# Kernel tuning notes

Measured on AMD Instinct MI355X. Metric: run time of the kernel, lower is better.

Reference implementation:

```python
import jax, jax.numpy as jnp
import numpy as np

# Model dims
H = 1024          # hidden_size
I = 2048          # intermediate_size
E = 8             # num_experts
IE = I // E       # expert_intermediate_size = 256
V = 100000        # vocab_size
B, S = 8, 2048


def _rowwise_quantize(x):
    """Dynamic per-row int8 quantization (faithful to dynamic_quantize_int8, per_channel=True).
    Returns quantized values kept in float32 (identical values to int8->float cast) and per-row scale."""
    max_vals = jnp.max(jnp.abs(x), axis=-1, keepdims=True)
    scale = jnp.maximum(max_vals / 127.0, 1e-8)
    x_q = jnp.clip(jnp.round(x / scale), -128.0, 127.0)
    return x_q, scale[..., 0]


def _quantize_weight(w):
    """Per-output-channel int8 quantization of a [K, N] weight (as in from_float)."""
    max_vals = jnp.max(jnp.abs(w), axis=0, keepdims=True)      # [1, N]
    scale = jnp.maximum(max_vals / 127.0, 1e-8)
    w_q = jnp.clip(jnp.round(w / scale), -128.0, 127.0).astype(jnp.int8)
    return w_q, scale[0]


def setup_inputs() -> dict:
    key = jax.random.key(0)
    ks = jax.random.split(key, 6)
    hidden_states = jax.random.normal(ks[0], (B, S, H), dtype=jnp.float32)
    token_ids = jax.random.randint(ks[1], (B, S), 0, V, dtype=jnp.int32)

    # Pre-quantized expert weights (int8) with per-output-channel fp32 scales.
    gate_w = jax.random.normal(ks[2], (E, H, IE), dtype=jnp.float32) * 0.02
    up_w = jax.random.normal(ks[3], (E, H, IE), dtype=jnp.float32) * 0.02
    down_w = jax.random.normal(ks[4], (E, IE, H), dtype=jnp.float32) * 0.02
    gate_q, gate_scale = jax.vmap(_quantize_weight)(gate_w)   # [E,H,IE] int8, [E,IE]
    up_q, up_scale = jax.vmap(_quantize_weight)(up_w)         # [E,H,IE] int8, [E,IE]
    down_q, down_scale = jax.vmap(_quantize_weight)(down_w)   # [E,IE,H] int8, [E,H]

    # Deterministic contiguous token->expert mapping (V divisible by E here).
    token_to_expert = jnp.minimum(jnp.arange(V, dtype=jnp.int32) // (V // E), E - 1)

    return {
        "hidden_states": hidden_states,
        "token_ids": token_ids,
        "gate_q": gate_q, "gate_scale": gate_scale,
        "up_q": up_q, "up_scale": up_scale,
        "down_q": down_q, "down_scale": down_scale,
        "token_to_expert": token_to_expert,
    }


def reference(hidden_states, token_ids, gate_q, gate_scale, up_q, up_scale,
              down_q, down_scale, token_to_expert):
    Bh, Sh, Hh = hidden_states.shape
    n_exp = gate_q.shape[0]
    vocab = token_to_expert.shape[0]

    tid = jnp.clip(token_ids, 0, vocab - 1)
    expert_ids = token_to_expert[tid].reshape(-1)             # [T]

    x = hidden_states.reshape(-1, Hh)                          # [T, H]
    # Per-row activation quantization is expert-independent -> do it once for all tokens.
    x_q, x_s = _rowwise_quantize(x)                            # [T,H], [T]

    gq = gate_q.astype(jnp.float32)
    uq = up_q.astype(jnp.float32)
    dq = down_q.astype(jnp.float32)

    out = jnp.zeros_like(x)
    for e in range(n_exp):  # small fixed expert count
        # fused quantize-GEMM: int8 matmul + per-row activation scale + per-col weight scale
        gate = (x_q @ gq[e]) * x_s[:, None] * gate_scale[e][None, :]   # [T, IE]
        up = (x_q @ uq[e]) * x_s[:, None] * up_scale[e][None, :]       # [T, IE]
        inter = jax.nn.silu(gate) * up
        i_q, i_s = _rowwise_quantize(inter)
        o = (i_q @ dq[e]) * i_s[:, None] * down_scale[e][None, :]      # [T, H]
        out = jnp.where((expert_ids == e)[:, None], o, out)
    return out.reshape(Bh, Sh, Hh)
```

## Files before the change

### kernel.cpp

```cpp
#include <hip/hip_runtime.h>
#include <hip/hip_bf16.h>

typedef int   int4v   __attribute__((ext_vector_type(4)));
typedef float float4v __attribute__((ext_vector_type(4)));

#define T_TOK 16384
#define TPAD  16448
#define HD    1024
#define IE    256
#define EN    8
#define VSZ   100000

#define M_OFF 16
#define M_TS1 25
#define M_TS2 34

#define XQ_OFF   0ull
#define IQ_OFF   16842752ull
#define PB1_OFF  21053440ull
#define PB2_OFF  25247744ull
#define PERM_OFF 27344896ull
#define XS_OFF   27410688ull
#define IS_OFF   27476480ull
#define META_OFF 27542272ull
#define BC_OFF   27542528ull
#define BB_OFF   27544576ull

__device__ __forceinline__ void gload16(const void* g, void* l) {
    __builtin_amdgcn_global_load_lds(
        (const __attribute__((address_space(1))) unsigned int*)g,
        (__attribute__((address_space(3))) unsigned int*)l,
        16, 0, 0);
}

__global__ void k_hist(const int* __restrict__ ids, const int* __restrict__ t2e,
                       int* __restrict__ bc) {
    __shared__ int h[EN];
    if (threadIdx.x < EN) h[threadIdx.x] = 0;
    __syncthreads();
    int t = blockIdx.x * 256 + threadIdx.x;
    int id = ids[t]; id = min(max(id, 0), VSZ - 1);
    atomicAdd(&h[t2e[id]], 1);
    __syncthreads();
    if (threadIdx.x < EN) bc[blockIdx.x * EN + threadIdx.x] = h[threadIdx.x];
}

__global__ __launch_bounds__(512) void k_scan(const int* __restrict__ bc,
                                              int* __restrict__ bbase,
                                              int* __restrict__ meta) {
    int e = threadIdx.x >> 6;
    int b = threadIdx.x & 63;
    int c = bc[b * EN + e];
    int inc = c;
    #pragma unroll
    for (int s = 1; s < 64; s <<= 1) {
        int v = __shfl_up(inc, s, 64);
        if (b >= s) inc += v;
    }
    int exc = inc - c;
    __shared__ int tot[EN];
    __shared__ int goff[EN];
    if (b == 63) tot[e] = inc;
    __syncthreads();
    if (threadIdx.x == 0) {
        int off = 0, t1 = 0, t2 = 0;
        meta[M_OFF] = 0; meta[M_TS1] = 0; meta[M_TS2] = 0;
        #pragma unroll
        for (int i = 0; i < EN; ++i) {
            goff[i] = off;
            int cc = tot[i];
            off += cc; t1 += (cc + 63) >> 6; t2 += (cc + 31) >> 5;
            meta[M_OFF + i + 1] = off;
            meta[M_TS1 + i + 1] = t1;
            meta[M_TS2 + i + 1] = t2;
        }
    }
    __syncthreads();
    bbase[b * EN + e] = goff[e] + exc;
}

__global__ void k_assign(const int* __restrict__ ids, const int* __restrict__ t2e,
                         const int* __restrict__ bbase, int* __restrict__ perm) {
    __shared__ int cur[EN];
    if (threadIdx.x < EN) cur[threadIdx.x] = bbase[blockIdx.x * EN + threadIdx.x];
    __syncthreads();
    int t = blockIdx.x * 256 + threadIdx.x;
    int id = ids[t]; id = min(max(id, 0), VSZ - 1);
    int e = t2e[id];
    int slot = atomicAdd(&cur[e], 1);
    perm[slot] = t;
}

__global__ __launch_bounds__(256) void k_repack(const int* __restrict__ gq,
                                                const int* __restrict__ uq,
                                                const int* __restrict__ dq,
                                                signed char* __restrict__ pb1,
                                                signed char* __restrict__ pb2) {
    int idx = blockIdx.x * 256 + threadIdx.x;
    if (idx < 262144) {
        int n = idx & 511, kc = (idx >> 9) & 63, e = idx >> 15;
        const int* src = (n < 256) ? gq + (((size_t)((e << 10) + (kc << 4)) << 8) + n)
                                   : uq + (((size_t)((e << 10) + (kc << 4)) << 8) + (n - 256));
        int4v pk;
        #pragma unroll
        for (int jj = 0; jj < 4; ++jj) {
            int b0 = src[(size_t)(jj * 4 + 0) << 8], b1 = src[(size_t)(jj * 4 + 1) << 8];
            int b2 = src[(size_t)(jj * 4 + 2) << 8], b3 = src[(size_t)(jj * 4 + 3) << 8];
            pk[jj] = (b0 & 255) | ((b1 & 255) << 8) | ((b2 & 255) << 16) | (b3 << 24);
        }
        *(int4v*)(pb1 + ((size_t)((((e << 6) + kc) << 9) + n) << 4)) = pk;
    } else {
        int j = idx - 262144;
        int n = j & 1023, kc = (j >> 10) & 15, e = j >> 14;
        const int* src = dq + (((size_t)((e << 8) + (kc << 4)) << 10) + n);
        int4v pk;
        #pragma unroll
        for (int jj = 0; jj < 4; ++jj) {
            int b0 = src[(size_t)(jj * 4 + 0) << 10], b1 = src[(size_t)(jj * 4 + 1) << 10];
            int b2 = src[(size_t)(jj * 4 + 2) << 10], b3 = src[(size_t)(jj * 4 + 3) << 10];
            pk[jj] = (b0 & 255) | ((b1 & 255) << 8) | ((b2 & 255) << 16) | (b3 << 24);
        }
        *(int4v*)(pb2 + ((size_t)((((e << 4) + kc) << 10) + n) << 4)) = pk;
    }
}

__global__ __launch_bounds__(256) void k_quant(const float* __restrict__ hidden,
                                               const int* __restrict__ perm,
                                               signed char* __restrict__ xq,
                                               float* __restrict__ xs) {
    int w = threadIdx.x >> 6, lane = threadIdx.x & 63;
    int slot = blockIdx.x * 4 + w;
    int token = perm[slot];
    const float* row = hidden + (size_t)token * HD;
    float v[16];
    #pragma unroll
    for (int j = 0; j < 4; ++j) {
        float4v f = *(const float4v*)(row + lane * 16 + j * 4);
        v[j*4+0] = f[0]; v[j*4+1] = f[1]; v[j*4+2] = f[2]; v[j*4+3] = f[3];
    }
    float mx = 0.0f;
    #pragma unroll
    for (int j = 0; j < 16; ++j) mx = fmaxf(mx, fabsf(v[j]));
    #pragma unroll
    for (int s = 1; s < 64; s <<= 1) mx = fmaxf(mx, __shfl_xor(mx, s, 64));
    float sc = fmaxf(mx / 127.0f, 1e-8f);
    if (lane == 0) xs[slot] = sc;
    int4v pk;
    #pragma unroll
    for (int j = 0; j < 4; ++j) {
        int b[4];
        #pragma unroll
        for (int u = 0; u < 4; ++u) {
            float t = rintf(v[j*4+u] / sc);
            t = fminf(fmaxf(t, -128.0f), 127.0f);
            b[u] = (int)t;
        }
        pk[j] = (b[0] & 255) | ((b[1] & 255) << 8) | ((b[2] & 255) << 16) | (b[3] << 24);
    }
    *(int4v*)(xq + (size_t)slot * HD + lane * 16) = pk;
}

__global__ __launch_bounds__(256, 2) void k_gemm1(const signed char* __restrict__ xq,
                                                  const signed char* __restrict__ pb1,
                                                  const float* __restrict__ xs,
                                                  const float* __restrict__ gsc,
                                                  const float* __restrict__ usc,
                                                  const int* __restrict__ meta,
                                                  signed char* __restrict__ iq,
                                                  float* __restrict__ isc) {
    int b = blockIdx.x;
    int e = -1, m0 = 0, gend = 0;
    #pragma unroll
    for (int i = 0; i < EN; ++i) {
        int s0 = meta[M_TS1 + i], s1 = meta[M_TS1 + i + 1];
        if (b >= s0 && b < s1) { e = i; m0 = meta[M_OFF + i] + ((b - s0) << 6); gend = meta[M_OFF + i + 1]; }
    }
    if (e < 0) return;
    const int w = threadIdx.x >> 6, lane = threadIdx.x & 63;
    const int q = lane >> 4, r = lane & 15;

    __shared__ signed char lB[2][32768];
    __shared__ signed char lA[2][4096];
    __shared__ float pmax[4][64];
    __shared__ float rsc[64];

    const signed char* pbe = pb1 + (size_t)e * (64 * 512 * 16);
    const int arow = (w << 4) + (lane >> 2);
    const int acq  = (lane & 3) ^ ((lane >> 2) & 3);
    const signed char* ga_base = xq + (size_t)(m0 + arow) * HD + (acq << 4);

    #define G1_STAGE(buf, kt)                                                          \
        {                                                                              \
            int kc0 = (kt) << 2;                                                       \
            _Pragma("unroll")                                                          \
            for (int j = 0; j < 8; ++j) {                                              \
                int n = ((j << 6) + lane) ^ ((w & 1) << 3);                            \
                gload16(pbe + (((size_t)(kc0 + w) * 512 + n) << 4),                    \
                        &lB[buf][((w << 3) + j) << 10]);                               \
            }                                                                          \
            gload16(ga_base + ((kt) << 6), &lA[buf][w << 10]);                         \
        }

    int4v zero = {0, 0, 0, 0};
    int4v accg[4][4], accu[4][4];
    #pragma unroll
    for (int mi = 0; mi < 4; ++mi)
        #pragma unroll
        for (int i = 0; i < 4; ++i) { accg[mi][i] = zero; accu[mi][i] = zero; }

    G1_STAGE(0, 0);
    for (int kt = 0; kt < 16; ++kt) {
        int cur = kt & 1;
        if (kt < 15) G1_STAGE(cur ^ 1, kt + 1);
        __syncthreads();
        int4v a[4];
        #pragma unroll
        for (int mi = 0; mi < 4; ++mi)
            a[mi] = *(const int4v*)&lA[cur][(((mi << 4) + r) << 6) + ((q ^ (r & 3)) << 4)];
        #pragma unroll
        for (int i = 0; i < 4; ++i) {
            int n = (w << 6) + (i << 4) + r;
            int sg = (q << 9) + (n ^ ((q & 1) << 3));
            int su = (q << 9) + ((n + 256) ^ ((q & 1) << 3));
            int4v bg = *(const int4v*)&lB[cur][sg << 4];
            int4v bu = *(const int4v*)&lB[cur][su << 4];
            #pragma unroll
            for (int mi = 0; mi < 4; ++mi) {
                accg[mi][i] = __builtin_amdgcn_mfma_i32_16x16x64_i8(a[mi], bg, accg[mi][i], 0, 0, 0);
                accu[mi][i] = __builtin_amdgcn_mfma_i32_16x16x64_i8(a[mi], bu, accu[mi][i], 0, 0, 0);
            }
        }
        __syncthreads();
    }
    #undef G1_STAGE

    float gs[4], us[4];
    #pragma unroll
    for (int i = 0; i < 4; ++i) {
        int n = (w << 6) + (i << 4) + r;
        gs[i] = gsc[e * IE + n];
        us[i] = usc[e * IE + n];
    }
    float xsr[4][4];
    #pragma unroll
    for (int mi = 0; mi < 4; ++mi)
        #pragma unroll
        for (int g = 0; g < 4; ++g)
            xsr[mi][g] = xs[m0 + mi * 16 + q * 4 + g];

    float inter[4][4][4];
    float pm[4][4];
    #pragma unroll
    for (int mi = 0; mi < 4; ++mi)
        #pragma unroll
        for (int g = 0; g < 4; ++g) {
            float mx = 0.0f;
            #pragma unroll
            for (int i = 0; i < 4; ++i) {
                float gv = (float)accg[mi][i][g] * xsr[mi][g] * gs[i];
                float uv = (float)accu[mi][i][g] * xsr[mi][g] * us[i];
                float sg = gv / (1.0f + expf(-gv));
                float vv = sg * uv;
                inter[mi][i][g] = vv;
                mx = fmaxf(mx, fabsf(vv));
            }
            #pragma unroll
            for (int s = 1; s < 16; s <<= 1) mx = fmaxf(mx, __shfl_xor(mx, s, 64));
            pm[mi][g] = mx;
        }

    if (r == 0) {
        #pragma unroll
        for (int mi = 0; mi < 4; ++mi)
            #pragma unroll
            for (int g = 0; g < 4; ++g)
                pmax[w][mi * 16 + q * 4 + g] = pm[mi][g];
    }
    __syncthreads();
    if (threadIdx.x < 64) {
        int row = threadIdx.x;
        float mx = fmaxf(fmaxf(pmax[0][row], pmax[1][row]), fmaxf(pmax[2][row], pmax[3][row]));
        float sc = fmaxf(mx / 127.0f, 1e-8f);
        rsc[row] = sc;
        if (m0 + row < gend) isc[m0 + row] = sc;
    }
    __syncthreads();
    #pragma unroll
    for (int mi = 0; mi < 4; ++mi)
        #pragma unroll
        for (int g = 0; g < 4; ++g) {
            int row = mi * 16 + q * 4 + g;
            int slot = m0 + row;
            if (slot < gend) {
                float sc = rsc[row];
                #pragma unroll
                for (int i = 0; i < 4; ++i) {
                    float t = rintf(inter[mi][i][g] / sc);
                    t = fminf(fmaxf(t, -128.0f), 127.0f);
                    iq[(size_t)slot * IE + (w << 6) + (i << 4) + r] = (signed char)(int)t;
                }
            }
        }
}

__global__ __launch_bounds__(256, 2) void k_gemm2(const signed char* __restrict__ iq,
                                                  const signed char* __restrict__ pb2,
                                                  const float* __restrict__ isc,
                                                  const float* __restrict__ dsc,
                                                  const int* __restrict__ meta,
                                                  const int* __restrict__ perm,
                                                  float* __restrict__ out) {
    int tile = blockIdx.x >> 1, nh = blockIdx.x & 1;
    int e = -1, m0 = 0, gend = 0;
    #pragma unroll
    for (int i = 0; i < EN; ++i) {
        int s0 = meta[M_TS2 + i], s1 = meta[M_TS2 + i + 1];
        if (tile >= s0 && tile < s1) { e = i; m0 = meta[M_OFF + i] + ((tile - s0) << 5); gend = meta[M_OFF + i + 1]; }
    }
    if (e < 0) return;
    const int w = threadIdx.x >> 6, lane = threadIdx.x & 63;
    const int q = lane >> 4, r = lane & 15;

    __shared__ signed char lB[2][32768];
    __shared__ signed char lA[2][2048];

    const signed char* pbe = pb2 + (size_t)e * (16 * 1024 * 16);
    const int arow = (w << 4) + (lane >> 2);
    const int acq  = (lane & 3) ^ ((lane >> 2) & 3);
    const signed char* ga_base = iq + (size_t)(m0 + arow) * IE + (acq << 4);

    #define G2_STAGE(buf, kt)                                                          \
        {                                                                              \
            int kc0 = (kt) << 2;                                                       \
            _Pragma("unroll")                                                          \
            for (int j = 0; j < 8; ++j) {                                              \
                int n = ((j << 6) + lane) ^ ((w & 1) << 3);                            \
                gload16(pbe + (((size_t)(kc0 + w) * 1024 + (nh << 9) + n) << 4),       \
                        &lB[buf][((w << 3) + j) << 10]);                               \
            }                                                                          \
            if (w < 2) gload16(ga_base + ((kt) << 6), &lA[buf][w << 10]);              \
        }

    int4v zero = {0, 0, 0, 0};
    int4v acc[2][8];
    #pragma unroll
    for (int mi = 0; mi < 2; ++mi)
        #pragma unroll
        for (int i = 0; i < 8; ++i) acc[mi][i] = zero;

    G2_STAGE(0, 0);
    for (int kt = 0; kt < 4; ++kt) {
        int cur = kt & 1;
        if (kt < 3) G2_STAGE(cur ^ 1, kt + 1);
        __syncthreads();
        int4v a[2];
        #pragma unroll
        for (int mi = 0; mi < 2; ++mi)
            a[mi] = *(const int4v*)&lA[cur][(((mi << 4) + r) << 6) + ((q ^ (r & 3)) << 4)];
        #pragma unroll
        for (int i = 0; i < 8; ++i) {
            int n = (w << 7) + (i << 4) + r;
            int sb = (q << 9) + (n ^ ((q & 1) << 3));
            int4v bb = *(const int4v*)&lB[cur][sb << 4];
            acc[0][i] = __builtin_amdgcn_mfma_i32_16x16x64_i8(a[0], bb, acc[0][i], 0, 0, 0);
            acc[1][i] = __builtin_amdgcn_mfma_i32_16x16x64_i8(a[1], bb, acc[1][i], 0, 0, 0);
        }
        __syncthreads();
    }
    #undef G2_STAGE

    float ds[8];
    #pragma unroll
    for (int i = 0; i < 8; ++i)
        ds[i] = dsc[e * HD + (nh << 9) + (w << 7) + (i << 4) + r];
    float isr[2][4]; int tok[2][4];
    #pragma unroll
    for (int mi = 0; mi < 2; ++mi)
        #pragma unroll
        for (int g = 0; g < 4; ++g) {
            int slot = m0 + mi * 16 + q * 4 + g;
            isr[mi][g] = isc[slot];
            tok[mi][g] = perm[slot];
        }
    #pragma unroll
    for (int mi = 0; mi < 2; ++mi)
        #pragma unroll
        for (int g = 0; g < 4; ++g) {
            int slot = m0 + mi * 16 + q * 4 + g;
            if (slot < gend) {
                float vs = isr[mi][g];
                size_t ob = (size_t)tok[mi][g] * HD + (nh << 9) + (w << 7) + r;
                #pragma unroll
                for (int i = 0; i < 8; ++i)
                    out[ob + (i << 4)] = (float)acc[mi][i][g] * vs * ds[i];
            }
        }
}

extern "C" void kernel_launch(void* const* d_in, const int* in_sizes, int n_in,
                              void* d_out, int out_size, void* d_ws, size_t ws_size,
                              hipStream_t stream) {
    const float* hidden = (const float*)d_in[0];
    const int*   ids    = (const int*)d_in[1];
    const int*   gq     = (const int*)d_in[2];
    const float* gsc    = (const float*)d_in[3];
    const int*   uq     = (const int*)d_in[4];
    const float* usc    = (const float*)d_in[5];
    const int*   dq     = (const int*)d_in[6];
    const float* dsc    = (const float*)d_in[7];
    const int*   t2e    = (const int*)d_in[8];
    float* out = (float*)d_out;

    char* ws = (char*)d_ws;
    signed char* xq  = (signed char*)(ws + XQ_OFF);
    signed char* iq  = (signed char*)(ws + IQ_OFF);
    signed char* pb1 = (signed char*)(ws + PB1_OFF);
    signed char* pb2 = (signed char*)(ws + PB2_OFF);
    int*   perm = (int*)(ws + PERM_OFF);
    float* xs   = (float*)(ws + XS_OFF);
    float* isc  = (float*)(ws + IS_OFF);
    int*   meta = (int*)(ws + META_OFF);
    int*   bc   = (int*)(ws + BC_OFF);
    int*   bbase= (int*)(ws + BB_OFF);

    k_hist<<<64, 256, 0, stream>>>(ids, t2e, bc);
    k_scan<<<1, 512, 0, stream>>>(bc, bbase, meta);
    k_assign<<<64, 256, 0, stream>>>(ids, t2e, bbase, perm);
    k_repack<<<1536, 256, 0, stream>>>(gq, uq, dq, pb1, pb2);
    k_quant<<<4096, 256, 0, stream>>>(hidden, perm, xq, xs);
    k_gemm1<<<264, 256, 0, stream>>>(xq, pb1, xs, gsc, usc, meta, iq, isc);
    k_gemm2<<<1040, 256, 0, stream>>>(iq, pb2, isc, dsc, meta, perm, out);
}
```

Measured before the change: 210.0 us.

## Fuse expert GEMMs into one kernel, merge routing and preprocessing launches

```diff
diff --git a/kernel.cpp b/kernel.cpp
--- a/kernel.cpp
+++ b/kernel.cpp
@@ -1,11 +1,9 @@
 #include <hip/hip_runtime.h>
-#include <hip/hip_bf16.h>
 
 typedef int   int4v   __attribute__((ext_vector_type(4)));
 typedef float float4v __attribute__((ext_vector_type(4)));
 
 #define T_TOK 16384
-#define TPAD  16448
 #define HD    1024
 #define IE    256
 #define EN    8
@@ -13,18 +11,13 @@
 
 #define M_OFF 16
 #define M_TS1 25
-#define M_TS2 34
 
 #define XQ_OFF   0ull
-#define IQ_OFF   16842752ull
 #define PB1_OFF  21053440ull
 #define PB2_OFF  25247744ull
 #define PERM_OFF 27344896ull
 #define XS_OFF   27410688ull
-#define IS_OFF   27476480ull
 #define META_OFF 27542272ull
-#define BC_OFF   27542528ull
-#define BB_OFF   27544576ull
 
 __device__ __forceinline__ void gload16(const void* g, void* l) {
     __builtin_amdgcn_global_load_lds(
@@ -33,141 +26,146 @@
         16, 0, 0);
 }
 
-__global__ void k_hist(const int* __restrict__ ids, const int* __restrict__ t2e,
-                       int* __restrict__ bc) {
-    __shared__ int h[EN];
-    if (threadIdx.x < EN) h[threadIdx.x] = 0;
-    __syncthreads();
-    int t = blockIdx.x * 256 + threadIdx.x;
-    int id = ids[t]; id = min(max(id, 0), VSZ - 1);
-    atomicAdd(&h[t2e[id]], 1);
-    __syncthreads();
-    if (threadIdx.x < EN) bc[blockIdx.x * EN + threadIdx.x] = h[threadIdx.x];
+__global__ __launch_bounds__(1024) void k_route(const int* __restrict__ ids,
+                                                const int* __restrict__ t2e,
+                                                int* __restrict__ perm,
+                                                int* __restrict__ meta) {
+    __shared__ int lbase[1024][EN];
+    __shared__ int wsum[16][EN];
+    __shared__ int goff[EN], tot[EN];
+    const int tid = threadIdx.x, lane = tid & 63, wv = tid >> 6;
+
+    #pragma unroll
+    for (int e = 0; e < EN; ++e) lbase[tid][e] = 0;
+    int e_of[16];
+    #pragma unroll
+    for (int i = 0; i < 16; ++i) {
+        int id = ids[tid * 16 + i];
+        id = min(max(id, 0), VSZ - 1);
+        int e = t2e[id];
+        e_of[i] = e;
+        lbase[tid][e]++;
+    }
+    #pragma unroll
+    for (int e = 0; e < EN; ++e) {
+        int v = lbase[tid][e];
+        int inc = v;
+        #pragma unroll
+        for (int s = 1; s < 64; s <<= 1) {
+            int u = __shfl_up(inc, s, 64);
+            if (lane >= s) inc += u;
+        }
+        lbase[tid][e] = inc - v;
+        if (lane == 63) wsum[wv][e] = inc;
+    }
+    __syncthreads();
+    if (tid < EN) {
+        int run = 0;
+        for (int w2 = 0; w2 < 16; ++w2) { int t = wsum[w2][tid]; wsum[w2][tid] = run; run += t; }
+        tot[tid] = run;
+    }
+    __syncthreads();
+    if (tid == 0) {
+        int off = 0, t1 = 0;
+        meta[M_OFF] = 0; meta[M_TS1] = 0;
+        #pragma unroll
+        for (int e = 0; e < EN; ++e) {
+            goff[e] = off;
+            off += tot[e];
+            t1 += (tot[e] + 63) >> 6;
+            meta[M_OFF + e + 1] = off;
+            meta[M_TS1 + e + 1] = t1;
+        }
+    }
+    __syncthreads();
+    #pragma unroll
+    for (int i = 0; i < 16; ++i) {
+        int e = e_of[i];
+        int c = lbase[tid][e];
+        lbase[tid][e] = c + 1;
+        perm[goff[e] + wsum[wv][e] + c] = tid * 16 + i;
+    }
 }
 
-__global__ __launch_bounds__(512) void k_scan(const int* __restrict__ bc,
-                                              int* __restrict__ bbase,
-                                              int* __restrict__ meta) {
-    int e = threadIdx.x >> 6;
-    int b = threadIdx.x & 63;
-    int c = bc[b * EN + e];
-    int inc = c;
-    #pragma unroll
-    for (int s = 1; s < 64; s <<= 1) {
-        int v = __shfl_up(inc, s, 64);
-        if (b >= s) inc += v;
-    }
-    int exc = inc - c;
-    __shared__ int tot[EN];
-    __shared__ int goff[EN];
-    if (b == 63) tot[e] = inc;
-    __syncthreads();
-    if (threadIdx.x == 0) {
-        int off = 0, t1 = 0, t2 = 0;
-        meta[M_OFF] = 0; meta[M_TS1] = 0; meta[M_TS2] = 0;
-        #pragma unroll
-        for (int i = 0; i < EN; ++i) {
-            goff[i] = off;
-            int cc = tot[i];
-            off += cc; t1 += (cc + 63) >> 6; t2 += (cc + 31) >> 5;
-            meta[M_OFF + i + 1] = off;
-            meta[M_TS1 + i + 1] = t1;
-            meta[M_TS2 + i + 1] = t2;
-        }
-    }
-    __syncthreads();
-    bbase[b * EN + e] = goff[e] + exc;
+__global__ __launch_bounds__(256) void k_pre(const float* __restrict__ hidden,
+                                             const int* __restrict__ gq,
+                                             const int* __restrict__ uq,
+                                             const int* __restrict__ dq,
+                                             signed char* __restrict__ xq,
+                                             float* __restrict__ xs,
+                                             signed char* __restrict__ pb1,
+                                             signed char* __restrict__ pb2) {
+    int b = blockIdx.x;
+    if (b < 4096) {
+        int w = threadIdx.x >> 6, lane = threadIdx.x & 63;
+        int token = (b << 2) + w;
+        const float* row = hidden + (size_t)token * HD;
+        float v[16];
+        #pragma unroll
+        for (int j = 0; j < 4; ++j) {
+            float4v f = *(const float4v*)(row + lane * 16 + j * 4);
+            v[j*4+0] = f[0]; v[j*4+1] = f[1]; v[j*4+2] = f[2]; v[j*4+3] = f[3];
+        }
+        float mx = 0.0f;
+        #pragma unroll
+        for (int j = 0; j < 16; ++j) mx = fmaxf(mx, fabsf(v[j]));
+        #pragma unroll
+        for (int s = 1; s < 64; s <<= 1) mx = fmaxf(mx, __shfl_xor(mx, s, 64));
+        float sc = fmaxf(mx / 127.0f, 1e-8f);
+        if (lane == 0) xs[token] = sc;
+        int4v pk;
+        #pragma unroll
+        for (int j = 0; j < 4; ++j) {
+            int bb[4];
+            #pragma unroll
+            for (int u = 0; u < 4; ++u) {
+                float t = rintf(v[j*4+u] / sc);
+                t = fminf(fmaxf(t, -128.0f), 127.0f);
+                bb[u] = (int)t;
+            }
+            pk[j] = (bb[0] & 255) | ((bb[1] & 255) << 8) | ((bb[2] & 255) << 16) | (bb[3] << 24);
+        }
+        *(int4v*)(xq + (size_t)token * HD + lane * 16) = pk;
+    } else {
+        int idx = (b - 4096) * 256 + threadIdx.x;
+        if (idx < 262144) {
+            int n = idx & 511, kc = (idx >> 9) & 63, e = idx >> 15;
+            const int* src = (n < 256) ? gq + (((size_t)((e << 10) + (kc << 4)) << 8) + n)
+                                       : uq + (((size_t)((e << 10) + (kc << 4)) << 8) + (n - 256));
+            int4v pk;
+            #pragma unroll
+            for (int jj = 0; jj < 4; ++jj) {
+                int b0 = src[(size_t)(jj * 4 + 0) << 8], b1 = src[(size_t)(jj * 4 + 1) << 8];
+                int b2 = src[(size_t)(jj * 4 + 2) << 8], b3 = src[(size_t)(jj * 4 + 3) << 8];
+                pk[jj] = (b0 & 255) | ((b1 & 255) << 8) | ((b2 & 255) << 16) | (b3 << 24);
+            }
+            *(int4v*)(pb1 + ((size_t)((((e << 6) + kc) << 9) + n) << 4)) = pk;
+        } else {
+            int j = idx - 262144;
+            int n = j & 1023, kc = (j >> 10) & 15, e = j >> 14;
+            const int* src = dq + (((size_t)((e << 8) + (kc << 4)) << 10) + n);
+            int4v pk;
+            #pragma unroll
+            for (int jj = 0; jj < 4; ++jj) {
+                int b0 = src[(size_t)(jj * 4 + 0) << 10], b1 = src[(size_t)(jj * 4 + 1) << 10];
+                int b2 = src[(size_t)(jj * 4 + 2) << 10], b3 = src[(size_t)(jj * 4 + 3) << 10];
+                pk[jj] = (b0 & 255) | ((b1 & 255) << 8) | ((b2 & 255) << 16) | (b3 << 24);
+            }
+            *(int4v*)(pb2 + ((size_t)((((e << 4) + kc) << 10) + n) << 4)) = pk;
+        }
+    }
 }
 
-__global__ void k_assign(const int* __restrict__ ids, const int* __restrict__ t2e,
-                         const int* __restrict__ bbase, int* __restrict__ perm) {
-    __shared__ int cur[EN];
-    if (threadIdx.x < EN) cur[threadIdx.x] = bbase[blockIdx.x * EN + threadIdx.x];
-    __syncthreads();
-    int t = blockIdx.x * 256 + threadIdx.x;
-    int id = ids[t]; id = min(max(id, 0), VSZ - 1);
-    int e = t2e[id];
-    int slot = atomicAdd(&cur[e], 1);
-    perm[slot] = t;
-}
-
-__global__ __launch_bounds__(256) void k_repack(const int* __restrict__ gq,
-                                                const int* __restrict__ uq,
-                                                const int* __restrict__ dq,
-                                                signed char* __restrict__ pb1,
-                                                signed char* __restrict__ pb2) {
-    int idx = blockIdx.x * 256 + threadIdx.x;
-    if (idx < 262144) {
-        int n = idx & 511, kc = (idx >> 9) & 63, e = idx >> 15;
-        const int* src = (n < 256) ? gq + (((size_t)((e << 10) + (kc << 4)) << 8) + n)
-                                   : uq + (((size_t)((e << 10) + (kc << 4)) << 8) + (n - 256));
-        int4v pk;
-        #pragma unroll
-        for (int jj = 0; jj < 4; ++jj) {
-            int b0 = src[(size_t)(jj * 4 + 0) << 8], b1 = src[(size_t)(jj * 4 + 1) << 8];
-            int b2 = src[(size_t)(jj * 4 + 2) << 8], b3 = src[(size_t)(jj * 4 + 3) << 8];
-            pk[jj] = (b0 & 255) | ((b1 & 255) << 8) | ((b2 & 255) << 16) | (b3 << 24);
-        }
-        *(int4v*)(pb1 + ((size_t)((((e << 6) + kc) << 9) + n) << 4)) = pk;
-    } else {
-        int j = idx - 262144;
-        int n = j & 1023, kc = (j >> 10) & 15, e = j >> 14;
-        const int* src = dq + (((size_t)((e << 8) + (kc << 4)) << 10) + n);
-        int4v pk;
-        #pragma unroll
-        for (int jj = 0; jj < 4; ++jj) {
-            int b0 = src[(size_t)(jj * 4 + 0) << 10], b1 = src[(size_t)(jj * 4 + 1) << 10];
-            int b2 = src[(size_t)(jj * 4 + 2) << 10], b3 = src[(size_t)(jj * 4 + 3) << 10];
-            pk[jj] = (b0 & 255) | ((b1 & 255) << 8) | ((b2 & 255) << 16) | (b3 << 24);
-        }
-        *(int4v*)(pb2 + ((size_t)((((e << 4) + kc) << 10) + n) << 4)) = pk;
-    }
-}
-
-__global__ __launch_bounds__(256) void k_quant(const float* __restrict__ hidden,
-                                               const int* __restrict__ perm,
-                                               signed char* __restrict__ xq,
-                                               float* __restrict__ xs) {
-    int w = threadIdx.x >> 6, lane = threadIdx.x & 63;
-    int slot = blockIdx.x * 4 + w;
-    int token = perm[slot];
-    const float* row = hidden + (size_t)token * HD;
-    float v[16];
-    #pragma unroll
-    for (int j = 0; j < 4; ++j) {
-        float4v f = *(const float4v*)(row + lane * 16 + j * 4);
-        v[j*4+0] = f[0]; v[j*4+1] = f[1]; v[j*4+2] = f[2]; v[j*4+3] = f[3];
-    }
-    float mx = 0.0f;
-    #pragma unroll
-    for (int j = 0; j < 16; ++j) mx = fmaxf(mx, fabsf(v[j]));
-    #pragma unroll
-    for (int s = 1; s < 64; s <<= 1) mx = fmaxf(mx, __shfl_xor(mx, s, 64));
-    float sc = fmaxf(mx / 127.0f, 1e-8f);
-    if (lane == 0) xs[slot] = sc;
-    int4v pk;
-    #pragma unroll
-    for (int j = 0; j < 4; ++j) {
-        int b[4];
-        #pragma unroll
-        for (int u = 0; u < 4; ++u) {
-            float t = rintf(v[j*4+u] / sc);
-            t = fminf(fmaxf(t, -128.0f), 127.0f);
-            b[u] = (int)t;
-        }
-        pk[j] = (b[0] & 255) | ((b[1] & 255) << 8) | ((b[2] & 255) << 16) | (b[3] << 24);
-    }
-    *(int4v*)(xq + (size_t)slot * HD + lane * 16) = pk;
-}
-
-__global__ __launch_bounds__(256, 2) void k_gemm1(const signed char* __restrict__ xq,
-                                                  const signed char* __restrict__ pb1,
-                                                  const float* __restrict__ xs,
-                                                  const float* __restrict__ gsc,
-                                                  const float* __restrict__ usc,
-                                                  const int* __restrict__ meta,
-                                                  signed char* __restrict__ iq,
-                                                  float* __restrict__ isc) {
+__global__ __launch_bounds__(256, 2) void k_mlp(const signed char* __restrict__ xq,
+                                                const signed char* __restrict__ pb1,
+                                                const signed char* __restrict__ pb2,
+                                                const float* __restrict__ xs,
+                                                const float* __restrict__ gsc,
+                                                const float* __restrict__ usc,
+                                                const float* __restrict__ dsc,
+                                                const int* __restrict__ meta,
+                                                const int* __restrict__ perm,
+                                                float* __restrict__ out) {
     int b = blockIdx.x;
     int e = -1, m0 = 0, gend = 0;
     #pragma unroll
@@ -179,15 +177,27 @@
     const int w = threadIdx.x >> 6, lane = threadIdx.x & 63;
     const int q = lane >> 4, r = lane & 15;
 
-    __shared__ signed char lB[2][32768];
-    __shared__ signed char lA[2][4096];
-    __shared__ float pmax[4][64];
-    __shared__ float rsc[64];
-
-    const signed char* pbe = pb1 + (size_t)e * (64 * 512 * 16);
+    __shared__ __align__(16) signed char lB[2][32768];
+    __shared__ __align__(16) signed char arena[16384];
+    float* pmax = (float*)(arena + 8192);
+    float* rsc  = (float*)(arena + 9216);
+    int*   ptok = (int*)(arena + 9472);
+
+    if (threadIdx.x < 64) ptok[threadIdx.x] = perm[min(m0 + (int)threadIdx.x, T_TOK - 1)];
+    __syncthreads();
+
+    int tokr[4][4];
+    #pragma unroll
+    for (int mi = 0; mi < 4; ++mi)
+        #pragma unroll
+        for (int g = 0; g < 4; ++g)
+            tokr[mi][g] = ptok[(mi << 4) + (q << 2) + g];
+
+    const signed char* pbe1 = pb1 + (size_t)e * (64 * 512 * 16);
+    const signed char* pbe2 = pb2 + (size_t)e * (16 * 1024 * 16);
     const int arow = (w << 4) + (lane >> 2);
     const int acq  = (lane & 3) ^ ((lane >> 2) & 3);
-    const signed char* ga_base = xq + (size_t)(m0 + arow) * HD + (acq << 4);
+    const signed char* ga_base = xq + (size_t)ptok[arow] * HD + (acq << 4);
 
     #define G1_STAGE(buf, kt)                                                          \
         {                                                                              \
@@ -195,10 +205,21 @@
             _Pragma("unroll")                                                          \
             for (int j = 0; j < 8; ++j) {                                              \
                 int n = ((j << 6) + lane) ^ ((w & 1) << 3);                            \
-                gload16(pbe + (((size_t)(kc0 + w) * 512 + n) << 4),                    \
+                gload16(pbe1 + (((size_t)(kc0 + w) * 512 + n) << 4),                   \
                         &lB[buf][((w << 3) + j) << 10]);                               \
             }                                                                          \
-            gload16(ga_base + ((kt) << 6), &lA[buf][w << 10]);                         \
+            gload16(ga_base + ((kt) << 6), arena + ((buf) << 12) + (w << 10));         \
+        }
+
+    #define G2_STAGE(buf, st)                                                          \
+        {                                                                              \
+            int kc0 = ((st) & 3) << 2; int nhs = (st) >> 2;                            \
+            _Pragma("unroll")                                                          \
+            for (int j = 0; j < 8; ++j) {                                              \
+                int n = ((j << 6) + lane) ^ ((w & 1) << 3);                            \
+                gload16(pbe2 + (((size_t)(kc0 + w) * 1024 + (nhs << 9) + n) << 4),     \
+                        &lB[buf][((w << 3) + j) << 10]);                               \
+            }                                                                          \
         }
 
     int4v zero = {0, 0, 0, 0};
@@ -216,7 +237,7 @@
         int4v a[4];
         #pragma unroll
         for (int mi = 0; mi < 4; ++mi)
-            a[mi] = *(const int4v*)&lA[cur][(((mi << 4) + r) << 6) + ((q ^ (r & 3)) << 4)];
+            a[mi] = *(const int4v*)&arena[(cur << 12) + ((((mi << 4) + r) << 6) + ((q ^ (r & 3)) << 4))];
         #pragma unroll
         for (int i = 0; i < 4; ++i) {
             int n = (w << 6) + (i << 4) + r;
@@ -234,6 +255,8 @@
     }
     #undef G1_STAGE
 
+    G2_STAGE(0, 0);
+
     float gs[4], us[4];
     #pragma unroll
     for (int i = 0; i < 4; ++i) {
@@ -246,7 +269,7 @@
     for (int mi = 0; mi < 4; ++mi)
         #pragma unroll
         for (int g = 0; g < 4; ++g)
-            xsr[mi][g] = xs[m0 + mi * 16 + q * 4 + g];
+            xsr[mi][g] = xs[tokr[mi][g]];
 
     float inter[4][4][4];
     float pm[4][4];
@@ -274,127 +297,85 @@
         for (int mi = 0; mi < 4; ++mi)
             #pragma unroll
             for (int g = 0; g < 4; ++g)
-                pmax[w][mi * 16 + q * 4 + g] = pm[mi][g];
+                pmax[(w << 6) + (mi << 4) + (q << 2) + g] = pm[mi][g];
     }
     __syncthreads();
     if (threadIdx.x < 64) {
         int row = threadIdx.x;
-        float mx = fmaxf(fmaxf(pmax[0][row], pmax[1][row]), fmaxf(pmax[2][row], pmax[3][row]));
-        float sc = fmaxf(mx / 127.0f, 1e-8f);
-        rsc[row] = sc;
-        if (m0 + row < gend) isc[m0 + row] = sc;
-    }
-    __syncthreads();
+        float mx = fmaxf(fmaxf(pmax[row], pmax[64 + row]), fmaxf(pmax[128 + row], pmax[192 + row]));
+        rsc[row] = fmaxf(mx / 127.0f, 1e-8f);
+    }
+    __syncthreads();
+    float rscr[4][4];
+    #pragma unroll
+    for (int mi = 0; mi < 4; ++mi)
+        #pragma unroll
+        for (int g = 0; g < 4; ++g)
+            rscr[mi][g] = rsc[(mi << 4) + (q << 2) + g];
+    __syncthreads();
+
     #pragma unroll
     for (int mi = 0; mi < 4; ++mi)
         #pragma unroll
         for (int g = 0; g < 4; ++g) {
-            int row = mi * 16 + q * 4 + g;
-            int slot = m0 + row;
-            if (slot < gend) {
-                float sc = rsc[row];
+            int row = (mi << 4) + (q << 2) + g;
+            float sc = rscr[mi][g];
+            #pragma unroll
+            for (int i = 0; i < 4; ++i) {
+                float t = rintf(inter[mi][i][g] / sc);
+                t = fminf(fmaxf(t, -128.0f), 127.0f);
+                arena[(row << 8) + ((((w << 2) + i) ^ (row & 3)) << 4) + r] = (signed char)(int)t;
+            }
+        }
+
+    int4v acc2[4][8];
+    for (int st = 0; st < 8; ++st) {
+        int cur = st & 1;
+        if (st < 7) G2_STAGE(cur ^ 1, st + 1);
+        if ((st & 3) == 0) {
+            #pragma unroll
+            for (int mi = 0; mi < 4; ++mi)
                 #pragma unroll
-                for (int i = 0; i < 4; ++i) {
-                    float t = rintf(inter[mi][i][g] / sc);
-                    t = fminf(fmaxf(t, -128.0f), 127.0f);
-                    iq[(size_t)slot * IE + (w << 6) + (i << 4) + r] = (signed char)(int)t;
-                }
-            }
-        }
-}
-
-__global__ __launch_bounds__(256, 2) void k_gemm2(const signed char* __restrict__ iq,
-                                                  const signed char* __restrict__ pb2,
-                                                  const float* __restrict__ isc,
-                                                  const float* __restrict__ dsc,
-                                                  const int* __restrict__ meta,
-                                                  const int* __restrict__ perm,
-                                                  float* __restrict__ out) {
-    int tile = blockIdx.x >> 1, nh = blockIdx.x & 1;
-    int e = -1, m0 = 0, gend = 0;
-    #pragma unroll
-    for (int i = 0; i < EN; ++i) {
-        int s0 = meta[M_TS2 + i], s1 = meta[M_TS2 + i + 1];
-        if (tile >= s0 && tile < s1) { e = i; m0 = meta[M_OFF + i] + ((tile - s0) << 5); gend = meta[M_OFF + i + 1]; }
-    }
-    if (e < 0) return;
-    const int w = threadIdx.x >> 6, lane = threadIdx.x & 63;
-    const int q = lane >> 4, r = lane & 15;
-
-    __shared__ signed char lB[2][32768];
-    __shared__ signed char lA[2][2048];
-
-    const signed char* pbe = pb2 + (size_t)e * (16 * 1024 * 16);
-    const int arow = (w << 4) + (lane >> 2);
-    const int acq  = (lane & 3) ^ ((lane >> 2) & 3);
-    const signed char* ga_base = iq + (size_t)(m0 + arow) * IE + (acq << 4);
-
-    #define G2_STAGE(buf, kt)                                                          \
-        {                                                                              \
-            int kc0 = (kt) << 2;                                                       \
-            _Pragma("unroll")                                                          \
-            for (int j = 0; j < 8; ++j) {                                              \
-                int n = ((j << 6) + lane) ^ ((w & 1) << 3);                            \
-                gload16(pbe + (((size_t)(kc0 + w) * 1024 + (nh << 9) + n) << 4),       \
-                        &lB[buf][((w << 3) + j) << 10]);                               \
-            }                                                                          \
-            if (w < 2) gload16(ga_base + ((kt) << 6), &lA[buf][w << 10]);              \
-        }
-
-    int4v zero = {0, 0, 0, 0};
-    int4v acc[2][8];
-    #pragma unroll
-    for (int mi = 0; mi < 2; ++mi)
-        #pragma unroll
-        for (int i = 0; i < 8; ++i) acc[mi][i] = zero;
-
-    G2_STAGE(0, 0);
-    for (int kt = 0; kt < 4; ++kt) {
-        int cur = kt & 1;
-        if (kt < 3) G2_STAGE(cur ^ 1, kt + 1);
+                for (int i = 0; i < 8; ++i) acc2[mi][i] = zero;
+        }
         __syncthreads();
-        int4v a[2];
-        #pragma unroll
-        for (int mi = 0; mi < 2; ++mi)
-            a[mi] = *(const int4v*)&lA[cur][(((mi << 4) + r) << 6) + ((q ^ (r & 3)) << 4)];
+        int4v a2[4];
+        #pragma unroll
+        for (int mi = 0; mi < 4; ++mi) {
+            int row2 = (mi << 4) + r;
+            a2[mi] = *(const int4v*)&arena[(row2 << 8) + (((((st & 3) << 2) + q) ^ (r & 3)) << 4)];
+        }
         #pragma unroll
         for (int i = 0; i < 8; ++i) {
             int n = (w << 7) + (i << 4) + r;
             int sb = (q << 9) + (n ^ ((q & 1) << 3));
             int4v bb = *(const int4v*)&lB[cur][sb << 4];
-            acc[0][i] = __builtin_amdgcn_mfma_i32_16x16x64_i8(a[0], bb, acc[0][i], 0, 0, 0);
-            acc[1][i] = __builtin_amdgcn_mfma_i32_16x16x64_i8(a[1], bb, acc[1][i], 0, 0, 0);
+            #pragma unroll
+            for (int mi = 0; mi < 4; ++mi)
+                acc2[mi][i] = __builtin_amdgcn_mfma_i32_16x16x64_i8(a2[mi], bb, acc2[mi][i], 0, 0, 0);
+        }
+        if ((st & 3) == 3) {
+            int nhs = st >> 2;
+            float ds[8];
+            #pragma unroll
+            for (int i = 0; i < 8; ++i)
+                ds[i] = dsc[e * HD + (nhs << 9) + (w << 7) + (i << 4) + r];
+            #pragma unroll
+            for (int mi = 0; mi < 4; ++mi)
+                #pragma unroll
+                for (int g = 0; g < 4; ++g) {
+                    int slot = m0 + (mi << 4) + (q << 2) + g;
+                    if (slot < gend) {
+                        size_t ob = (size_t)tokr[mi][g] * HD + (nhs << 9) + (w << 7) + r;
+                        #pragma unroll
+                        for (int i = 0; i < 8; ++i)
+                            out[ob + (i << 4)] = (float)acc2[mi][i][g] * rscr[mi][g] * ds[i];
+                    }
+                }
         }
         __syncthreads();
     }
     #undef G2_STAGE
-
-    float ds[8];
-    #pragma unroll
-    for (int i = 0; i < 8; ++i)
-        ds[i] = dsc[e * HD + (nh << 9) + (w << 7) + (i << 4) + r];
-    float isr[2][4]; int tok[2][4];
-    #pragma unroll
-    for (int mi = 0; mi < 2; ++mi)
-        #pragma unroll
-        for (int g = 0; g < 4; ++g) {
-            int slot = m0 + mi * 16 + q * 4 + g;
-            isr[mi][g] = isc[slot];
-            tok[mi][g] = perm[slot];
-        }
-    #pragma unroll
-    for (int mi = 0; mi < 2; ++mi)
-        #pragma unroll
-        for (int g = 0; g < 4; ++g) {
-            int slot = m0 + mi * 16 + q * 4 + g;
-            if (slot < gend) {
-                float vs = isr[mi][g];
-                size_t ob = (size_t)tok[mi][g] * HD + (nh << 9) + (w << 7) + r;
-                #pragma unroll
-                for (int i = 0; i < 8; ++i)
-                    out[ob + (i << 4)] = (float)acc[mi][i][g] * vs * ds[i];
-            }
-        }
 }
 
 extern "C" void kernel_launch(void* const* d_in, const int* in_sizes, int n_in,
@@ -413,21 +394,13 @@
 
     char* ws = (char*)d_ws;
     signed char* xq  = (signed char*)(ws + XQ_OFF);
-    signed char* iq  = (signed char*)(ws + IQ_OFF);
     signed char* pb1 = (signed char*)(ws + PB1_OFF);
     signed char* pb2 = (signed char*)(ws + PB2_OFF);
     int*   perm = (int*)(ws + PERM_OFF);
     float* xs   = (float*)(ws + XS_OFF);
-    float* isc  = (float*)(ws + IS_OFF);
     int*   meta = (int*)(ws + META_OFF);
-    int*   bc   = (int*)(ws + BC_OFF);
-    int*   bbase= (int*)(ws + BB_OFF);
-
-    k_hist<<<64, 256, 0, stream>>>(ids, t2e, bc);
-    k_scan<<<1, 512, 0, stream>>>(bc, bbase, meta);
-    k_assign<<<64, 256, 0, stream>>>(ids, t2e, bbase, perm);
-    k_repack<<<1536, 256, 0, stream>>>(gq, uq, dq, pb1, pb2);
-    k_quant<<<4096, 256, 0, stream>>>(hidden, perm, xq, xs);
-    k_gemm1<<<264, 256, 0, stream>>>(xq, pb1, xs, gsc, usc, meta, iq, isc);
-    k_gemm2<<<1040, 256, 0, stream>>>(iq, pb2, isc, dsc, meta, perm, out);
+
+    k_route<<<1, 1024, 0, stream>>>(ids, t2e, perm, meta);
+    k_pre<<<5632, 256, 0, stream>>>(hidden, gq, uq, dq, xq, xs, pb1, pb2);
+    k_mlp<<<264, 256, 0, stream>>>(xq, pb1, pb2, xs, gsc, usc, dsc, meta, perm, out);
 }
```

After: 233.8 us. 11.3% more time.
